# Kernel optimization log

Measured on AMD Instinct MI355X. Metric: run time of the kernel, lower is better.

Reference implementation:

```python
import jax, jax.numpy as jnp
import numpy as np

# Instant-NGP 2D hash-grid hyperparameters (hard-coded in the flax module)
L = 16          # levels
T = 1 << 20     # table size per level (power of 2)
F = 2           # features per entry
N_MIN = 16      # coarsest resolution; growth factor b == 2 given N_max = 2**19
HASH_PRIME_Y = 2654435761  # pi2 from Instant-NGP spatial hash

_CORNER_OFFS = np.array([[0, 0], [0, 1], [1, 0], [1, 1]], dtype=np.uint32)  # 2D cell corners


def hashgrid_encode(uv, tables):
    """uv: [N,2] in [0,1]; tables: [L,T,F]. Returns [N, L*F]."""
    offs = jnp.asarray(_CORNER_OFFS)            # [4,2] uint32
    offs_b = offs.astype(bool)
    feats = []
    for l in range(L):
        res = N_MIN * (2 ** l)                  # 16, 32, ..., 2**19 (static)
        pos = uv * res                          # [N,2]
        pf = jnp.floor(pos)
        w = pos - pf                            # [N,2] interpolation weights
        c = pf.astype(jnp.uint32)               # [N,2] cell corner
        corner = c[:, None, :] + offs[None]     # [N,4,2]
        if (res + 1) ** 2 <= T:
            # level fits densely in the table: row-major linear index
            idx = corner[..., 0] + corner[..., 1] * jnp.uint32(res + 1)
        else:
            # spatial hash: xor of coordinate * prime, masked to table size
            idx = corner[..., 0] ^ (corner[..., 1] * jnp.uint32(HASH_PRIME_Y))
            idx = idx & jnp.uint32(T - 1)
        f = tables[l][idx]                      # gather: [N,4,F]
        # bilinear weights per corner: prod_d (off_d ? w_d : 1-w_d)
        cw = jnp.prod(jnp.where(offs_b[None], w[:, None, :], 1.0 - w[:, None, :]), axis=-1)  # [N,4]
        feats.append(jnp.einsum('nc,ncf->nf', cw, f))  # [N,F]
    return jnp.concatenate(feats, axis=-1)      # [N, L*F]


def setup_inputs() -> dict:
    key = jax.random.key(0)
    ks = jax.random.split(key, 8)
    N = 1 << 20
    uv = jax.random.uniform(ks[0], (N, 2), dtype=jnp.float32)
    # Instant-NGP init: uniform in [-1e-4, 1e-4]
    tables = jax.random.uniform(ks[1], (L, T, F), dtype=jnp.float32, minval=-1e-4, maxval=1e-4)
    d_in = L * F  # 32
    lecun = lambda k, fi, fo: jax.random.normal(k, (fi, fo), dtype=jnp.float32) / jnp.sqrt(jnp.float32(fi))
    return {
        'uv': uv,
        'tables': tables,
        'w1': lecun(ks[2], d_in, 128), 'b1': jnp.zeros((128,), jnp.float32),
        'w2': lecun(ks[3], 128, 128),  'b2': jnp.zeros((128,), jnp.float32),
        'w3': lecun(ks[4], 128, 3),    'b3': jnp.zeros((3,), jnp.float32),
    }


def reference(uv, tables, w1, b1, w2, b2, w3, b3):
    x = hashgrid_encode(uv, tables)             # [N, 32]
    x = jax.nn.relu(x @ w1 + b1)                # [N, 128]
    x = jax.nn.relu(x @ w2 + b2)                # [N, 128]
    rgb = jax.nn.sigmoid(x @ w3 + b3)           # [N, 3]
    return rgb
```

## Files before the change

### kernel.cpp

```cpp
#include <hip/hip_runtime.h>


#define T_SIZE  (1u << 20)
#define HASH_Y  2654435761u
#define NLVL    16
#define MAXPTS  (1u << 20)

typedef __bf16 bf16x8 __attribute__((ext_vector_type(8)));
typedef float f32x4 __attribute__((ext_vector_type(4)));
typedef unsigned short u16x8 __attribute__((ext_vector_type(8)));
typedef unsigned short u16x4 __attribute__((ext_vector_type(4)));

__device__ unsigned int g_tbl[NLVL * T_SIZE];
__device__ unsigned int g_feat[NLVL * MAXPTS];

static __device__ __forceinline__ unsigned short f2bf(float f) {
    union { float f; unsigned u; } v; v.f = f;
    unsigned u = v.u;
    u += 0x7fffu + ((u >> 16) & 1u);
    return (unsigned short)(u >> 16);
}

static __device__ __forceinline__ unsigned packbf(float a, float b) {
    return (unsigned)f2bf(a) | ((unsigned)f2bf(b) << 16);
}

static __device__ __forceinline__ float bflo(unsigned p) {
    union { unsigned u; float f; } v; v.u = p << 16; return v.f;
}
static __device__ __forceinline__ float bfhi(unsigned p) {
    union { unsigned u; float f; } v; v.u = p & 0xffff0000u; return v.f;
}

static __device__ __forceinline__ f32x4 mfma16(u16x8 a, u16x8 b, f32x4 c) {
    return __builtin_amdgcn_mfma_f32_16x16x32_bf16(
        __builtin_bit_cast(bf16x8, a), __builtin_bit_cast(bf16x8, b), c, 0, 0, 0);
}

__global__ __launch_bounds__(256)
void ngp_pack(const float* __restrict__ tables)
{
    unsigned i = (blockIdx.x * 256u + threadIdx.x) * 4u;
    const float4* s = (const float4*)(tables + (size_t)i * 2);
    float4 a = s[0], b = s[1];
    uint4 o;
    o.x = packbf(a.x, a.y);
    o.y = packbf(a.z, a.w);
    o.z = packbf(b.x, b.y);
    o.w = packbf(b.z, b.w);
    *(uint4*)(g_tbl + i) = o;
}

__global__ __launch_bounds__(256)
void ngp_encode(const float* __restrict__ uv, int npts, int bpl)
{
    const int bid = blockIdx.x;
    const int lvl = bid / bpl;
    const int blk = bid - lvl * bpl;
    const int base = (blk << 10) + (threadIdx.x << 2);
    if (base >= npts) return;

    const unsigned res = 16u << lvl;
    const float fres = (float)res;
    const unsigned rp1 = res + 1u;
    const unsigned mask = T_SIZE - 1u;
    const bool dense = lvl < 6;
    const unsigned* __restrict__ tl = g_tbl + (size_t)lvl * T_SIZE;

    const float4* u4 = (const float4*)(uv + (size_t)base * 2);
    float4 ua = u4[0], ub = u4[1];
    float pxa[4] = {ua.x, ua.z, ub.x, ub.z};
    float pya[4] = {ua.y, ua.w, ub.y, ub.w};

    unsigned i00[4], i01[4], i10[4], i11[4];
    float wx[4], wy[4];
#pragma unroll
    for (int u = 0; u < 4; ++u) {
        float px = pxa[u] * fres, py = pya[u] * fres;
        float fx = floorf(px), fy = floorf(py);
        wx[u] = px - fx; wy[u] = py - fy;
        unsigned cx = (unsigned)fx, cy = (unsigned)fy;
        unsigned hy0 = cy * HASH_Y, hy1 = (cy + 1u) * HASH_Y;
        i00[u] = dense ? (cx + cy * rp1)              : ((cx ^ hy0) & mask);
        i01[u] = dense ? (cx + (cy + 1u) * rp1)       : ((cx ^ hy1) & mask);
        i10[u] = dense ? (cx + 1u + cy * rp1)         : (((cx + 1u) ^ hy0) & mask);
        i11[u] = dense ? (cx + 1u + (cy + 1u) * rp1)  : (((cx + 1u) ^ hy1) & mask);
    }
    unsigned e00[4], e01[4], e10[4], e11[4];
#pragma unroll
    for (int u = 0; u < 4; ++u) {
        e00[u] = tl[i00[u]];
        e01[u] = tl[i01[u]];
        e10[u] = tl[i10[u]];
        e11[u] = tl[i11[u]];
    }
    __builtin_amdgcn_sched_barrier(0);
    unsigned pk[4];
#pragma unroll
    for (int u = 0; u < 4; ++u) {
        float w00 = (1.f - wx[u]) * (1.f - wy[u]);
        float w01 = (1.f - wx[u]) * wy[u];
        float w10 = wx[u] * (1.f - wy[u]);
        float w11 = wx[u] * wy[u];
        float g0 = w00 * bflo(e00[u]) + w01 * bflo(e01[u]) + w10 * bflo(e10[u]) + w11 * bflo(e11[u]);
        float g1 = w00 * bfhi(e00[u]) + w01 * bfhi(e01[u]) + w10 * bfhi(e10[u]) + w11 * bfhi(e11[u]);
        pk[u] = packbf(g0, g1);
    }
    *(uint4*)(g_feat + (size_t)lvl * npts + base) = make_uint4(pk[0], pk[1], pk[2], pk[3]);
}

__global__ __launch_bounds__(256, 2)
void ngp_mlp(const float* __restrict__ w1, const float* __restrict__ b1,
             const float* __restrict__ w2, const float* __restrict__ b2,
             const float* __restrict__ w3, const float* __restrict__ b3,
             float* __restrict__ out, int npts)
{
    __shared__ __align__(16) unsigned short w2T[128 * 136];
    __shared__ __align__(16) unsigned short hbuf[4 * 16 * 136];
    __shared__ float b1s[128], b2s[128];

    const int tid = threadIdx.x;
    for (int e = tid; e < 128 * 128; e += 256) {
        int i = e >> 7, o = e & 127;
        w2T[o * 136 + i] = f2bf(w2[e]);
    }
    if (tid < 128) { b1s[tid] = b1[tid]; b2s[tid] = b2[tid]; }
    __syncthreads();

    const int lane = tid & 63;
    const int wv = tid >> 6;
    const int lanelo = lane & 15;
    const int quad = lane >> 4;

    u16x8 a1[8];
#pragma unroll
    for (int mt = 0; mt < 8; ++mt)
#pragma unroll
        for (int j = 0; j < 8; ++j)
            a1[mt][j] = f2bf(w1[(quad * 8 + j) * 128 + mt * 16 + lanelo]);

    u16x8 a3[4];
#pragma unroll
    for (int ks = 0; ks < 4; ++ks)
#pragma unroll
        for (int j = 0; j < 8; ++j) {
            int k = ks * 32 + quad * 8 + j;
            a3[ks][j] = (lanelo < 3) ? f2bf(w3[k * 3 + lanelo]) : (unsigned short)0;
        }
    float b3r0 = b3[0], b3r1 = b3[1], b3r2 = b3[2];

    const int NT = npts >> 4;
    const int nwaves = gridDim.x * 4;
    const int gwave = blockIdx.x * 4 + wv;
    const int niter = (NT + nwaves - 1) / nwaves;

    unsigned short* hp = hbuf + (wv * 16 + lanelo) * 136;
    const int lvlbase = quad << 2;

    unsigned c0 = 0, c1 = 0, c2 = 0, c3 = 0;
    if (gwave < NT) {
        int pt0 = (gwave << 4) + lanelo;
        c0 = g_feat[(size_t)(lvlbase + 0) * npts + pt0];
        c1 = g_feat[(size_t)(lvlbase + 1) * npts + pt0];
        c2 = g_feat[(size_t)(lvlbase + 2) * npts + pt0];
        c3 = g_feat[(size_t)(lvlbase + 3) * npts + pt0];
    }

    for (int it = 0; it < niter; ++it) {
        int tile = gwave + it * nwaves;
        bool act = tile < NT;
        int pt = (tile << 4) + lanelo;

        if (act) {
            u16x8 xb;
            xb[0] = (unsigned short)(c0 & 0xffffu); xb[1] = (unsigned short)(c0 >> 16);
            xb[2] = (unsigned short)(c1 & 0xffffu); xb[3] = (unsigned short)(c1 >> 16);
            xb[4] = (unsigned short)(c2 & 0xffffu); xb[5] = (unsigned short)(c2 >> 16);
            xb[6] = (unsigned short)(c3 & 0xffffu); xb[7] = (unsigned short)(c3 >> 16);

            int tn = tile + nwaves;
            if (tn < NT) {
                int ptn = (tn << 4) + lanelo;
                c0 = g_feat[(size_t)(lvlbase + 0) * npts + ptn];
                c1 = g_feat[(size_t)(lvlbase + 1) * npts + ptn];
                c2 = g_feat[(size_t)(lvlbase + 2) * npts + ptn];
                c3 = g_feat[(size_t)(lvlbase + 3) * npts + ptn];
            }

            f32x4 z = {0.f, 0.f, 0.f, 0.f};
            f32x4 d[8];
#pragma unroll
            for (int mt = 0; mt < 8; ++mt) d[mt] = mfma16(a1[mt], xb, z);
#pragma unroll
            for (int mt = 0; mt < 8; ++mt) {
                u16x4 pk;
#pragma unroll
                for (int r = 0; r < 4; ++r) {
                    float hv = d[mt][r] + b1s[mt * 16 + quad * 4 + r];
                    pk[r] = f2bf(fmaxf(hv, 0.f));
                }
                *(u16x4*)(hp + mt * 16 + quad * 4) = pk;
            }
        }
        __syncthreads();
        if (act) {
            f32x4 z = {0.f, 0.f, 0.f, 0.f};
            f32x4 e[8];
#pragma unroll
            for (int mt = 0; mt < 8; ++mt) e[mt] = z;
#pragma unroll
            for (int ks = 0; ks < 4; ++ks) {
                u16x8 bb = *(const u16x8*)(hp + ks * 32 + quad * 8);
#pragma unroll
                for (int mt = 0; mt < 8; ++mt) {
                    u16x8 aa = *(const u16x8*)(w2T + (mt * 16 + lanelo) * 136 + ks * 32 + quad * 8);
                    e[mt] = mfma16(aa, bb, e[mt]);
                }
            }
#pragma unroll
            for (int mt = 0; mt < 8; ++mt) {
                u16x4 pk;
#pragma unroll
                for (int r = 0; r < 4; ++r) {
                    float hv = e[mt][r] + b2s[mt * 16 + quad * 4 + r];
                    pk[r] = f2bf(fmaxf(hv, 0.f));
                }
                *(u16x4*)(hp + mt * 16 + quad * 4) = pk;
            }
        }
        __syncthreads();
        if (act) {
            f32x4 o3 = {0.f, 0.f, 0.f, 0.f};
#pragma unroll
            for (int ks = 0; ks < 4; ++ks) {
                u16x8 bb = *(const u16x8*)(hp + ks * 32 + quad * 8);
                o3 = mfma16(a3[ks], bb, o3);
            }
            if (quad == 0) {
                float* op = out + (size_t)pt * 3;
                op[0] = 1.f / (1.f + expf(-(o3[0] + b3r0)));
                op[1] = 1.f / (1.f + expf(-(o3[1] + b3r1)));
                op[2] = 1.f / (1.f + expf(-(o3[2] + b3r2)));
            }
        }
    }
}

extern "C" void kernel_launch(void* const* d_in, const int* in_sizes, int n_in,
                              void* d_out, int out_size, void* d_ws, size_t ws_size,
                              hipStream_t stream) {
    const float* uv     = (const float*)d_in[0];
    const float* tables = (const float*)d_in[1];
    const float* w1     = (const float*)d_in[2];
    const float* b1     = (const float*)d_in[3];
    const float* w2     = (const float*)d_in[4];
    const float* b2     = (const float*)d_in[5];
    const float* w3     = (const float*)d_in[6];
    const float* b3     = (const float*)d_in[7];
    float* out = (float*)d_out;
    int npts = in_sizes[0] / 2;

    hipLaunchKernelGGL(ngp_pack, dim3((NLVL * T_SIZE) / 1024), dim3(256), 0, stream,
                       tables);

    int bpl = (npts + 1023) >> 10;
    hipLaunchKernelGGL(ngp_encode, dim3(NLVL * bpl), dim3(256), 0, stream,
                       uv, npts, bpl);

    hipLaunchKernelGGL(ngp_mlp, dim3(2048), dim3(256), 0, stream,
                       w1, b1, w2, b2, w3, b3, out, npts);
}
```

Baseline: 522.2 us.

## Pair adjacent grid corners into 64-bit loads to halve encode gathers

Dense levels now go through a new precomputed bf16 table in which each entry also holds its x+1 neighbour, so each point needs two 8-byte gathers instead of four 4-byte ones. Hash levels exploit the fact that cx and cx+1 hash to the same aligned pair of entries when cx is even. They load aligned uint2 pairs and only fetch the second pair when cx is odd, picking the right halves from the parity bits. The bf16 pack now skips the dense levels, and encode gets an occupancy hint. The cost is an extra small pre-pass kernel, more selection logic, and a divergent branch on odd cx.

```diff
diff --git a/kernel.cpp b/kernel.cpp
--- a/kernel.cpp
+++ b/kernel.cpp
@@ -5,13 +5,17 @@
 #define HASH_Y  2654435761u
 #define NLVL    16
 #define MAXPTS  (1u << 20)
+#define DP_TOTAL 351462
 
 typedef __bf16 bf16x8 __attribute__((ext_vector_type(8)));
 typedef float f32x4 __attribute__((ext_vector_type(4)));
 typedef unsigned short u16x8 __attribute__((ext_vector_type(8)));
 typedef unsigned short u16x4 __attribute__((ext_vector_type(4)));
 
+__constant__ int DP_OFF[7] = {0, 289, 1378, 5603, 22244, 88293, DP_TOTAL};
+
 __device__ unsigned int g_tbl[NLVL * T_SIZE];
+__device__ uint2        g_dp[DP_TOTAL];
 __device__ unsigned int g_feat[NLVL * MAXPTS];
 
 static __device__ __forceinline__ unsigned short f2bf(float f) {
@@ -40,7 +44,7 @@
 __global__ __launch_bounds__(256)
 void ngp_pack(const float* __restrict__ tables)
 {
-    unsigned i = (blockIdx.x * 256u + threadIdx.x) * 4u;
+    unsigned i = 6u * T_SIZE + (blockIdx.x * 256u + threadIdx.x) * 4u;
     const float4* s = (const float4*)(tables + (size_t)i * 2);
     float4 a = s[0], b = s[1];
     uint4 o;
@@ -52,6 +56,25 @@
 }
 
 __global__ __launch_bounds__(256)
+void ngp_dense(const float* __restrict__ tables)
+{
+    int idx = blockIdx.x * 256 + threadIdx.x;
+    if (idx >= DP_TOTAL) return;
+    int lvl = 0;
+#pragma unroll
+    for (int l = 1; l < 6; ++l) if (idx >= DP_OFF[l]) lvl = l;
+    int loc = idx - DP_OFF[lvl];
+    unsigned rp1 = (16u << lvl) + 1u;
+    unsigned cy = (unsigned)loc / rp1;
+    unsigned cx = (unsigned)loc - cy * rp1;
+    const float2* t2 = (const float2*)tables + (size_t)lvl * T_SIZE;
+    float2 a = t2[cy * rp1 + cx];
+    unsigned cx1 = (cx + 1u < rp1) ? cx + 1u : cx;
+    float2 b = t2[cy * rp1 + cx1];
+    g_dp[idx] = make_uint2(packbf(a.x, a.y), packbf(b.x, b.y));
+}
+
+__global__ __launch_bounds__(256, 6)
 void ngp_encode(const float* __restrict__ uv, int npts, int bpl)
 {
     const int bid = blockIdx.x;
@@ -62,39 +85,91 @@
 
     const unsigned res = 16u << lvl;
     const float fres = (float)res;
-    const unsigned rp1 = res + 1u;
     const unsigned mask = T_SIZE - 1u;
-    const bool dense = lvl < 6;
-    const unsigned* __restrict__ tl = g_tbl + (size_t)lvl * T_SIZE;
 
     const float4* u4 = (const float4*)(uv + (size_t)base * 2);
     float4 ua = u4[0], ub = u4[1];
     float pxa[4] = {ua.x, ua.z, ub.x, ub.z};
     float pya[4] = {ua.y, ua.w, ub.y, ub.w};
 
-    unsigned i00[4], i01[4], i10[4], i11[4];
     float wx[4], wy[4];
-#pragma unroll
-    for (int u = 0; u < 4; ++u) {
-        float px = pxa[u] * fres, py = pya[u] * fres;
-        float fx = floorf(px), fy = floorf(py);
-        wx[u] = px - fx; wy[u] = py - fy;
-        unsigned cx = (unsigned)fx, cy = (unsigned)fy;
-        unsigned hy0 = cy * HASH_Y, hy1 = (cy + 1u) * HASH_Y;
-        i00[u] = dense ? (cx + cy * rp1)              : ((cx ^ hy0) & mask);
-        i01[u] = dense ? (cx + (cy + 1u) * rp1)       : ((cx ^ hy1) & mask);
-        i10[u] = dense ? (cx + 1u + cy * rp1)         : (((cx + 1u) ^ hy0) & mask);
-        i11[u] = dense ? (cx + 1u + (cy + 1u) * rp1)  : (((cx + 1u) ^ hy1) & mask);
-    }
-    unsigned e00[4], e01[4], e10[4], e11[4];
-#pragma unroll
-    for (int u = 0; u < 4; ++u) {
-        e00[u] = tl[i00[u]];
-        e01[u] = tl[i01[u]];
-        e10[u] = tl[i10[u]];
-        e11[u] = tl[i11[u]];
-    }
-    __builtin_amdgcn_sched_barrier(0);
+    unsigned v00[4], v10[4], v01[4], v11[4];
+
+    if (lvl < 6) {
+        const unsigned rp1 = res + 1u;
+        const uint2* __restrict__ dp = g_dp + DP_OFF[lvl];
+        unsigned i0[4];
+#pragma unroll
+        for (int u = 0; u < 4; ++u) {
+            float px = pxa[u] * fres, py = pya[u] * fres;
+            float fx = floorf(px), fy = floorf(py);
+            wx[u] = px - fx; wy[u] = py - fy;
+            unsigned cx = (unsigned)fx, cy = (unsigned)fy;
+            i0[u] = cy * rp1 + cx;
+        }
+        uint2 q0[4], q1[4];
+#pragma unroll
+        for (int u = 0; u < 4; ++u) {
+            q0[u] = dp[i0[u]];
+            q1[u] = dp[i0[u] + rp1];
+        }
+        __builtin_amdgcn_sched_barrier(0);
+#pragma unroll
+        for (int u = 0; u < 4; ++u) {
+            v00[u] = q0[u].x; v10[u] = q0[u].y;
+            v01[u] = q1[u].x; v11[u] = q1[u].y;
+        }
+    } else {
+        const unsigned* __restrict__ tl = g_tbl + (size_t)lvl * T_SIZE;
+        unsigned p00[4], p01[4], p10[4], p11[4], oddb[4], c0b[4];
+#pragma unroll
+        for (int u = 0; u < 4; ++u) {
+            float px = pxa[u] * fres, py = pya[u] * fres;
+            float fx = floorf(px), fy = floorf(py);
+            wx[u] = px - fx; wy[u] = py - fy;
+            unsigned cx = (unsigned)fx, cy = (unsigned)fy;
+            unsigned odd = cx & 1u;
+            unsigned cxe = cx & ~1u;
+            unsigned cxn = (cx + 1u) & ~1u;
+            unsigned hy0 = cy * HASH_Y, hy1 = hy0 + HASH_Y;
+            p00[u] = ((cxe ^ hy0) & mask) & ~1u;
+            p01[u] = ((cxe ^ hy1) & mask) & ~1u;
+            p10[u] = ((cxn ^ hy0) & mask) & ~1u;
+            p11[u] = ((cxn ^ hy1) & mask) & ~1u;
+            oddb[u] = odd;
+            c0b[u] = cy & 1u;
+        }
+        uint2 q00[4], q01[4], r10[4], r11[4];
+#pragma unroll
+        for (int u = 0; u < 4; ++u) {
+            q00[u] = *(const uint2*)(tl + p00[u]);
+            q01[u] = *(const uint2*)(tl + p01[u]);
+            r10[u] = make_uint2(0u, 0u);
+            r11[u] = make_uint2(0u, 0u);
+        }
+#pragma unroll
+        for (int u = 0; u < 4; ++u) {
+            if (oddb[u]) {
+                r10[u] = *(const uint2*)(tl + p10[u]);
+                r11[u] = *(const uint2*)(tl + p11[u]);
+            }
+        }
+        __builtin_amdgcn_sched_barrier(0);
+#pragma unroll
+        for (int u = 0; u < 4; ++u) {
+            unsigned c0 = c0b[u], od = oddb[u];
+            unsigned sL0 = c0 ^ od;
+            unsigned c1 = c0 ^ 1u;
+            unsigned sL1 = c1 ^ od;
+            uint2 h10 = od ? r10[u] : q00[u];
+            uint2 h11 = od ? r11[u] : q01[u];
+            v00[u] = sL0 ? q00[u].y : q00[u].x;
+            v10[u] = sL0 ? h10.x   : h10.y;
+            v01[u] = sL1 ? q01[u].y : q01[u].x;
+            v11[u] = sL1 ? h11.x   : h11.y;
+        }
+    }
+
     unsigned pk[4];
 #pragma unroll
     for (int u = 0; u < 4; ++u) {
@@ -102,8 +177,8 @@
         float w01 = (1.f - wx[u]) * wy[u];
         float w10 = wx[u] * (1.f - wy[u]);
         float w11 = wx[u] * wy[u];
-        float g0 = w00 * bflo(e00[u]) + w01 * bflo(e01[u]) + w10 * bflo(e10[u]) + w11 * bflo(e11[u]);
-        float g1 = w00 * bfhi(e00[u]) + w01 * bfhi(e01[u]) + w10 * bfhi(e10[u]) + w11 * bfhi(e11[u]);
+        float g0 = w00 * bflo(v00[u]) + w01 * bflo(v01[u]) + w10 * bflo(v10[u]) + w11 * bflo(v11[u]);
+        float g1 = w00 * bfhi(v00[u]) + w01 * bfhi(v01[u]) + w10 * bfhi(v10[u]) + w11 * bfhi(v11[u]);
         pk[u] = packbf(g0, g1);
     }
     *(uint4*)(g_feat + (size_t)lvl * npts + base) = make_uint4(pk[0], pk[1], pk[2], pk[3]);
@@ -260,7 +335,9 @@
     float* out = (float*)d_out;
     int npts = in_sizes[0] / 2;
 
-    hipLaunchKernelGGL(ngp_pack, dim3((NLVL * T_SIZE) / 1024), dim3(256), 0, stream,
+    hipLaunchKernelGGL(ngp_pack, dim3((10u * T_SIZE) / 1024), dim3(256), 0, stream,
+                       tables);
+    hipLaunchKernelGGL(ngp_dense, dim3((DP_TOTAL + 255) / 256), dim3(256), 0, stream,
                        tables);
 
     int bpl = (npts + 1023) >> 10;
```

Measured after the change: 500.8 us. -4.1%, faster.
